# Kernel optimization log

Hardware: AMD Instinct MI355X
Metric: run time of the kernel (lower is better)

The kernel has to match this reference:

```python
import jax, jax.numpy as jnp
import numpy as np

HID, HEADS, FFN = 2048, 16, 8192
HEAD_DIM = HID // HEADS
B, S = 2, 2048
EPS = 1e-5


def setup_inputs() -> dict:
    key = jax.random.key(0)
    ks = jax.random.split(key, 12)
    s = 0.02
    x = jax.random.normal(ks[0], (B, S, HID), dtype=jnp.float32)
    # additive causal mask: 0 on/below diagonal, -inf-like above
    neg = jnp.float32(-1e9)
    causal = jnp.where(jnp.tril(jnp.ones((S, S), dtype=bool)), 0.0, neg)
    mask = causal[None, None, :, :].astype(jnp.float32)
    return {
        "x": x,
        "mask": mask,
        "ln1_w": jnp.ones((HID,), jnp.float32),
        "ln1_b": jnp.zeros((HID,), jnp.float32),
        "q_w": jax.random.normal(ks[1], (HID, HID), jnp.float32) * s,
        "k_w": jax.random.normal(ks[2], (HID, HID), jnp.float32) * s,
        "v_w": jax.random.normal(ks[3], (HID, HID), jnp.float32) * s,
        "o_w": jax.random.normal(ks[4], (HID, HID), jnp.float32) * s,
        "ln2_w": jnp.ones((HID,), jnp.float32),
        "ln2_b": jnp.zeros((HID,), jnp.float32),
        "w1_w": jax.random.normal(ks[5], (FFN, HID), jnp.float32) * s,
        "w1_b": jnp.zeros((FFN,), jnp.float32),
        "wg_w": jax.random.normal(ks[6], (FFN, HID), jnp.float32) * s,
        "w2_w": jax.random.normal(ks[7], (HID, FFN), jnp.float32) * s,
        "w2_b": jnp.zeros((HID,), jnp.float32),
    }


def _layernorm(x, w, b):
    mu = jnp.mean(x, axis=-1, keepdims=True)
    var = jnp.mean(jnp.square(x - mu), axis=-1, keepdims=True)
    return (x - mu) * jax.lax.rsqrt(var + EPS) * w + b


def reference(x, mask, ln1_w, ln1_b, q_w, k_w, v_w, o_w,
              ln2_w, ln2_b, w1_w, w1_b, wg_w, w2_w, w2_b):
    b, s, _ = x.shape
    # --- attention sublayer ---
    h = _layernorm(x, ln1_w, ln1_b)
    def split_heads(y):  # [b,s,hid] -> [b,H,s,d]
        return y.reshape(b, s, HEADS, HEAD_DIM).transpose(0, 2, 1, 3)
    q = split_heads(h @ q_w.T)
    k = split_heads(h @ k_w.T)
    v = split_heads(h @ v_w.T)
    scale = jnp.sqrt(jnp.float32(HEAD_DIM))
    scores = jnp.einsum('bhqd,bhkd->bhqk', q, k) / scale + mask
    weights = jax.nn.softmax(scores, axis=-1)
    attn = jnp.einsum('bhqk,bhkd->bhqd', weights, v)
    attn = attn.transpose(0, 2, 1, 3).reshape(b, s, HID)
    x = x + attn @ o_w.T
    # --- SwiGLU FFN sublayer ---
    h2 = _layernorm(x, ln2_w, ln2_b)
    ff = jax.nn.silu(h2 @ w1_w.T + w1_b) * (h2 @ wg_w.T)
    x = x + ff @ w2_w.T + w2_b
    return x
```

## Files before the change

### kernel.cpp

```cpp
#include <hip/hip_runtime.h>
#include <cstdint>
#include <cstddef>

#define HIDN 2048
#define NROWS 4096
#define FFND 8192
#define SEQ 2048
#define QKVN 6144

typedef __attribute__((ext_vector_type(8))) __bf16 bf16x8;
typedef __attribute__((ext_vector_type(4))) float f32x4;

__device__ __forceinline__ unsigned short f2b(float f) {
    union { float f; unsigned u; } v; v.f = f;
    unsigned r = v.u + 0x7fffu + ((v.u >> 16) & 1u);
    return (unsigned short)(r >> 16);
}
__device__ __forceinline__ float b2f(unsigned short h) {
    union { unsigned u; float f; } v; v.u = ((unsigned)h) << 16; return v.f;
}
__device__ __forceinline__ void gload16(const void* g, void* lds) {
    __builtin_amdgcn_global_load_lds(
        (const __attribute__((address_space(1))) void*)g,
        (__attribute__((address_space(3))) void*)lds, 16, 0, 0);
}

__global__ __launch_bounds__(256) void convall_kernel(
    const float* __restrict__ s0, const float* __restrict__ s1,
    const float* __restrict__ s2, const float* __restrict__ s3,
    const float* __restrict__ s4, const float* __restrict__ s5,
    const float* __restrict__ s6, unsigned short* __restrict__ dst) {
    const int M1 = 1 << 20;
    int i = blockIdx.x * 256 + threadIdx.x;
    const float* src; int rel;
    if      (i <  1 * M1) { src = s0; rel = i;          }
    else if (i <  2 * M1) { src = s1; rel = i - 1 * M1; }
    else if (i <  3 * M1) { src = s2; rel = i - 2 * M1; }
    else if (i <  4 * M1) { src = s3; rel = i - 3 * M1; }
    else if (i <  8 * M1) { src = s4; rel = i - 4 * M1; }
    else if (i < 12 * M1) { src = s5; rel = i - 8 * M1; }
    else                  { src = s6; rel = i - 12 * M1; }
    float4 v = ((const float4*)src)[rel];
    ushort4 o;
    o.x = f2b(v.x); o.y = f2b(v.y); o.z = f2b(v.z); o.w = f2b(v.w);
    ((ushort4*)dst)[i] = o;
}

__global__ __launch_bounds__(256) void ln_kernel(const float* __restrict__ x,
                                                 const float* __restrict__ w,
                                                 const float* __restrict__ b,
                                                 unsigned short* __restrict__ out) {
    int row = blockIdx.x, tid = threadIdx.x;
    const float4* xr = (const float4*)(x + (size_t)row * HIDN);
    float4 a0 = xr[tid], a1 = xr[tid + 256];
    float s  = a0.x + a0.y + a0.z + a0.w + a1.x + a1.y + a1.z + a1.w;
    float s2 = a0.x*a0.x + a0.y*a0.y + a0.z*a0.z + a0.w*a0.w
             + a1.x*a1.x + a1.y*a1.y + a1.z*a1.z + a1.w*a1.w;
#pragma unroll
    for (int i = 1; i < 64; i <<= 1) { s += __shfl_xor(s, i); s2 += __shfl_xor(s2, i); }
    __shared__ float red[8];
    if ((tid & 63) == 0) { red[tid >> 6] = s; red[4 + (tid >> 6)] = s2; }
    __syncthreads();
    s  = red[0] + red[1] + red[2] + red[3];
    s2 = red[4] + red[5] + red[6] + red[7];
    float mu  = s * (1.0f / HIDN);
    float var = s2 * (1.0f / HIDN) - mu * mu;
    float rstd = rsqrtf(var + 1e-5f);
    const float4* wv = (const float4*)w;
    const float4* bv = (const float4*)b;
    float4 w0 = wv[tid], w1 = wv[tid + 256], b0 = bv[tid], b1 = bv[tid + 256];
    ushort4 o0, o1;
    o0.x = f2b((a0.x - mu) * rstd * w0.x + b0.x);
    o0.y = f2b((a0.y - mu) * rstd * w0.y + b0.y);
    o0.z = f2b((a0.z - mu) * rstd * w0.z + b0.z);
    o0.w = f2b((a0.w - mu) * rstd * w0.w + b0.w);
    o1.x = f2b((a1.x - mu) * rstd * w1.x + b1.x);
    o1.y = f2b((a1.y - mu) * rstd * w1.y + b1.y);
    o1.z = f2b((a1.z - mu) * rstd * w1.z + b1.z);
    o1.w = f2b((a1.w - mu) * rstd * w1.w + b1.w);
    ushort4* orow = (ushort4*)(out + (size_t)row * HIDN);
    orow[tid] = o0; orow[tid + 256] = o1;
}

template <int EPI>
__global__ __launch_bounds__(512)
void gemm256(const unsigned short* __restrict__ A, const unsigned short* __restrict__ Bw,
             int M, int N, int K, int tiles_n, float scale,
             const float* __restrict__ bias, const float* __restrict__ resf,
             const unsigned short* __restrict__ aux,
             float* __restrict__ outf, unsigned short* __restrict__ outb) {
    __shared__ unsigned short lds[4][2][8192];
    int tid = threadIdx.x;
    int wave = tid >> 6, lane = tid & 63;
    int lrow = lane & 15, quad = lane >> 4;
    int wm = wave >> 2, wn = wave & 3;
    int nchunk = tiles_n >> 3;
    int xcd = blockIdx.x & 7;
    int pxi = blockIdx.x >> 3;
    int bn = xcd * nchunk + pxi % nchunk;
    int bm = pxi / nchunk;

    f32x4 acc[8][4];
#pragma unroll
    for (int i = 0; i < 8; i++)
#pragma unroll
        for (int j = 0; j < 4; j++) acc[i][j] = f32x4{0.f, 0.f, 0.f, 0.f};

    int srow = wave * 16 + (lane >> 2);
    int scol = (lane & 3) * 8;
    const unsigned short* Ag = A + (size_t)(bm * 256 + srow) * K + scol;
    const unsigned short* Bg = Bw + (size_t)(bn * 256 + srow) * K + scol;
    const int NT = K >> 5;

    auto stage = [&](int slab, int part) {
        const unsigned short* g = part ? Bg : Ag;
        unsigned short* lb = &lds[slab & 3][part][wave * 512];
        size_t koff = (size_t)slab << 5;
        gload16(g + koff, lb);
        gload16(g + koff + (size_t)128 * K, lb + 4096);
    };

    stage(0, 0); stage(0, 1);
    stage(1, 0); stage(1, 1);
    stage(2, 0); stage(2, 1);
    asm volatile("s_waitcnt vmcnt(8)" ::: "memory");
    __builtin_amdgcn_s_barrier();
    asm volatile("" ::: "memory");

#pragma unroll 1
    for (int t = 0; t < NT; ++t) {
        const unsigned short* Abuf = &lds[t & 3][0][0];
        const unsigned short* Bbuf = &lds[t & 3][1][0];
        bf16x8 bfr[4], afr[4];
#pragma unroll
        for (int ni = 0; ni < 4; ni++)
            bfr[ni] = *(const bf16x8*)&Bbuf[(wn * 64 + ni * 16 + lrow) * 32 + quad * 8];
#pragma unroll
        for (int mi = 0; mi < 4; mi++)
            afr[mi] = *(const bf16x8*)&Abuf[(wm * 128 + mi * 16 + lrow) * 32 + quad * 8];
        if (t + 3 < NT) stage(t + 3, 0);
        __builtin_amdgcn_s_barrier();
        asm volatile("s_waitcnt lgkmcnt(0)" ::: "memory");
        __builtin_amdgcn_s_setprio(1);
#pragma unroll
        for (int mi = 0; mi < 4; mi++)
#pragma unroll
            for (int ni = 0; ni < 4; ni++)
                acc[mi][ni] = __builtin_amdgcn_mfma_f32_16x16x32_bf16(afr[mi], bfr[ni], acc[mi][ni], 0, 0, 0);
        __builtin_amdgcn_s_setprio(0);
        __builtin_amdgcn_s_barrier();
        asm volatile("" ::: "memory");
#pragma unroll
        for (int mi = 0; mi < 4; mi++)
            afr[mi] = *(const bf16x8*)&Abuf[(wm * 128 + 64 + mi * 16 + lrow) * 32 + quad * 8];
        if (t + 3 < NT) {
            stage(t + 3, 1);
            asm volatile("s_waitcnt vmcnt(8)" ::: "memory");
        } else if (t + 2 < NT) {
            asm volatile("s_waitcnt vmcnt(4)" ::: "memory");
        } else if (t + 1 < NT) {
            asm volatile("s_waitcnt vmcnt(0)" ::: "memory");
        }
        __builtin_amdgcn_s_barrier();
        asm volatile("s_waitcnt lgkmcnt(0)" ::: "memory");
        __builtin_amdgcn_s_setprio(1);
#pragma unroll
        for (int mi = 0; mi < 4; mi++)
#pragma unroll
            for (int ni = 0; ni < 4; ni++)
                acc[4 + mi][ni] = __builtin_amdgcn_mfma_f32_16x16x32_bf16(afr[mi], bfr[ni], acc[4 + mi][ni], 0, 0, 0);
        __builtin_amdgcn_s_setprio(0);
        __builtin_amdgcn_s_barrier();
        asm volatile("" ::: "memory");
    }

    int row0 = bm * 256 + wm * 128, col0 = bn * 256 + wn * 64;
#pragma unroll
    for (int mi8 = 0; mi8 < 8; mi8++) {
        int rbase = row0 + (mi8 >> 2) * 64 + (mi8 & 3) * 16 + quad * 4;
#pragma unroll
        for (int ni = 0; ni < 4; ni++) {
            int c = col0 + ni * 16 + lrow;
#pragma unroll
            for (int r = 0; r < 4; r++) {
                size_t idx = (size_t)(rbase + r) * N + c;
                float vv = acc[mi8][ni][r];
                if constexpr (EPI == 0) {
                    outb[idx] = f2b(vv * scale);
                } else if constexpr (EPI == 1) {
                    outf[idx] = vv + resf[idx];
                } else if constexpr (EPI == 2) {
                    outb[idx] = f2b(vv + bias[c]);
                } else if constexpr (EPI == 3) {
                    float av = b2f(aux[idx]);
                    float sl = av / (1.f + __expf(-av));
                    outb[idx] = f2b(sl * vv);
                } else if constexpr (EPI == 4) {
                    outf[idx] = vv + bias[c] + resf[idx];
                } else if constexpr (EPI == 5) {
                    outb[idx] = f2b(vv * (c < HIDN ? scale : 1.0f));
                }
            }
        }
    }
    (void)M;
}

__global__ __launch_bounds__(256)
void attn_kernel(const unsigned short* __restrict__ qkv, unsigned short* __restrict__ o) {
    int bh = blockIdx.x;
    int qt = 31 - blockIdx.y;
    int b = bh >> 4, h = bh & 15;
    int tid = threadIdx.x, wave = tid >> 6, lane = tid & 63;
    int lrow = lane & 15, quad = lane >> 4;
    int q0 = qt * 64;
    size_t base = ((size_t)b * SEQ) * QKVN + h * 128;
    const unsigned short* qp0 = qkv + base;
    const unsigned short* kp0 = qkv + base + HIDN;
    const unsigned short* vp0 = qkv + base + 2 * HIDN;
    size_t obase = ((size_t)b * SEQ) * HIDN + h * 128;

    __shared__ unsigned short Ksm[64 * 136];
    __shared__ unsigned short VTsm[128 * 72];
    __shared__ unsigned short Psm[4 * 16 * 72];

    bf16x8 qf[4];
    {
        const unsigned short* qp = qp0 + (size_t)(q0 + wave * 16 + lrow) * QKVN + quad * 8;
#pragma unroll
        for (int kc = 0; kc < 4; kc++) qf[kc] = *(const bf16x8*)(qp + kc * 32);
    }

    f32x4 oacc[8];
#pragma unroll
    for (int i = 0; i < 8; i++) oacc[i] = f32x4{0.f, 0.f, 0.f, 0.f};
    float m_run[4], l_run[4];
    int rowg[4];
#pragma unroll
    for (int r = 0; r < 4; r++) {
        m_run[r] = -1e30f; l_run[r] = 0.f;
        rowg[r] = q0 + wave * 16 + quad * 4 + r;
    }

    for (int kt = 0; kt <= qt; ++kt) {
        {
            int r = tid >> 2, cc = (tid & 3) * 32;
            const uint4* src = (const uint4*)(kp0 + (size_t)(kt * 64 + r) * QKVN + cc);
            uint4* dst = (uint4*)&Ksm[r * 136 + cc];
            dst[0] = src[0]; dst[1] = src[1]; dst[2] = src[2]; dst[3] = src[3];
        }
        {
            int kv = (tid >> 3) * 2, d0 = (tid & 7) * 16;
            const unsigned short* vp = vp0 + (size_t)(kt * 64 + kv) * QKVN + d0;
            unsigned short va[16], vb[16];
            *(uint4*)&va[0] = ((const uint4*)vp)[0];
            *(uint4*)&va[8] = ((const uint4*)vp)[1];
            *(uint4*)&vb[0] = ((const uint4*)(vp + QKVN))[0];
            *(uint4*)&vb[8] = ((const uint4*)(vp + QKVN))[1];
#pragma unroll
            for (int i = 0; i < 16; i++) {
                unsigned pair = (unsigned)va[i] | ((unsigned)vb[i] << 16);
                *(unsigned*)&VTsm[(d0 + i) * 72 + kv] = pair;
            }
        }
        __syncthreads();

        f32x4 sacc[4];
#pragma unroll
        for (int ns = 0; ns < 4; ns++) sacc[ns] = f32x4{0.f, 0.f, 0.f, 0.f};
#pragma unroll
        for (int ns = 0; ns < 4; ns++) {
            const unsigned short* kb = &Ksm[(ns * 16 + lrow) * 136 + quad * 8];
#pragma unroll
            for (int kc = 0; kc < 4; kc++) {
                bf16x8 kf = *(const bf16x8*)(kb + kc * 32);
                sacc[ns] = __builtin_amdgcn_mfma_f32_16x16x32_bf16(qf[kc], kf, sacc[ns], 0, 0, 0);
            }
        }
#pragma unroll
        for (int ns = 0; ns < 4; ns++) {
            int colg = kt * 64 + ns * 16 + lrow;
#pragma unroll
            for (int r = 0; r < 4; r++)
                if (colg > rowg[r]) sacc[ns][r] = -1e30f;
        }
        float mnew[4], alpha[4], rsum[4];
#pragma unroll
        for (int r = 0; r < 4; r++) {
            float mv = fmaxf(fmaxf(sacc[0][r], sacc[1][r]), fmaxf(sacc[2][r], sacc[3][r]));
#pragma unroll
            for (int off = 1; off < 16; off <<= 1) mv = fmaxf(mv, __shfl_xor(mv, off));
            mnew[r] = fmaxf(m_run[r], mv);
            alpha[r] = __expf(m_run[r] - mnew[r]);
            rsum[r] = 0.f;
        }
#pragma unroll
        for (int ns = 0; ns < 4; ns++)
#pragma unroll
            for (int r = 0; r < 4; r++) {
                float p = __expf(sacc[ns][r] - mnew[r]);
                sacc[ns][r] = p;
                rsum[r] += p;
            }
#pragma unroll
        for (int r = 0; r < 4; r++) {
#pragma unroll
            for (int off = 1; off < 16; off <<= 1) rsum[r] += __shfl_xor(rsum[r], off);
            l_run[r] = l_run[r] * alpha[r] + rsum[r];
            m_run[r] = mnew[r];
        }
#pragma unroll
        for (int nc = 0; nc < 8; nc++)
#pragma unroll
            for (int r = 0; r < 4; r++) oacc[nc][r] *= alpha[r];

        unsigned short* pw = &Psm[wave * 16 * 72];
#pragma unroll
        for (int ns = 0; ns < 4; ns++)
#pragma unroll
            for (int r = 0; r < 4; r++)
                pw[(quad * 4 + r) * 72 + ns * 16 + lrow] = f2b(sacc[ns][r]);
        asm volatile("s_waitcnt lgkmcnt(0)" ::: "memory");
        bf16x8 pf[2];
#pragma unroll
        for (int kc = 0; kc < 2; kc++)
            pf[kc] = *(const bf16x8*)&pw[lrow * 72 + kc * 32 + quad * 8];
#pragma unroll
        for (int nc = 0; nc < 8; nc++) {
#pragma unroll
            for (int kc = 0; kc < 2; kc++) {
                bf16x8 vf = *(const bf16x8*)&VTsm[(nc * 16 + lrow) * 72 + kc * 32 + quad * 8];
                oacc[nc] = __builtin_amdgcn_mfma_f32_16x16x32_bf16(pf[kc], vf, oacc[nc], 0, 0, 0);
            }
        }
        __syncthreads();
    }

    float inv[4];
#pragma unroll
    for (int r = 0; r < 4; r++) inv[r] = 1.f / l_run[r];
#pragma unroll
    for (int nc = 0; nc < 8; nc++) {
#pragma unroll
        for (int r = 0; r < 4; r++) {
            int srow = q0 + wave * 16 + quad * 4 + r;
            o[obase + (size_t)srow * HIDN + nc * 16 + lrow] = f2b(oacc[nc][r] * inv[r]);
        }
    }
}

extern "C" void kernel_launch(void* const* d_in, const int* in_sizes, int n_in,
                              void* d_out, int out_size, void* d_ws, size_t ws_size,
                              hipStream_t stream) {
    const float* x    = (const float*)d_in[0];
    const float* ln1w = (const float*)d_in[2];
    const float* ln1b = (const float*)d_in[3];
    const float* qw   = (const float*)d_in[4];
    const float* kw   = (const float*)d_in[5];
    const float* vw   = (const float*)d_in[6];
    const float* ow   = (const float*)d_in[7];
    const float* ln2w = (const float*)d_in[8];
    const float* ln2b = (const float*)d_in[9];
    const float* w1w  = (const float*)d_in[10];
    const float* w1bias = (const float*)d_in[11];
    const float* wgw  = (const float*)d_in[12];
    const float* w2w  = (const float*)d_in[13];
    const float* w2bias = (const float*)d_in[14];
    float* out = (float*)d_out;

    char* ws = (char*)d_ws;
    const size_t MB = 1ull << 20;
    unsigned short* wall  = (unsigned short*)(ws + 0 * MB);
    unsigned short* qkvwb = (unsigned short*)(ws + 0 * MB);
    unsigned short* owb  = (unsigned short*)(ws + 24 * MB);
    unsigned short* w1wb = (unsigned short*)(ws + 32 * MB);
    unsigned short* wgwb = (unsigned short*)(ws + 64 * MB);
    unsigned short* w2wb = (unsigned short*)(ws + 96 * MB);
    unsigned short* a1   = (unsigned short*)(ws + 128 * MB);
    unsigned short* hbuf = (unsigned short*)(ws + 128 * MB);
    unsigned short* qkvb = (unsigned short*)(ws + 144 * MB);
    unsigned short* attnb= (unsigned short*)(ws + 192 * MB);
    unsigned short* h2   = (unsigned short*)(ws + 208 * MB);
    float*          x1   = out;

    convall_kernel<<<65536, 256, 0, stream>>>(qw, kw, vw, ow, w1w, wgw, w2w, wall);

    ln_kernel<<<NROWS, 256, 0, stream>>>(x, ln1w, ln1b, hbuf);

    const float qscale = 0.08838834764831845f;
    gemm256<5><<<dim3(16 * 24), 512, 0, stream>>>(hbuf, qkvwb, NROWS, QKVN, HIDN, 24, qscale,
                                                  nullptr, nullptr, nullptr, nullptr, qkvb);
    attn_kernel<<<dim3(32, 32), 256, 0, stream>>>(qkvb, attnb);
    gemm256<1><<<dim3(16 * 8), 512, 0, stream>>>(attnb, owb, NROWS, HIDN, HIDN, 8, 1.0f,
                                                 nullptr, x, nullptr, x1, nullptr);
    ln_kernel<<<NROWS, 256, 0, stream>>>(x1, ln2w, ln2b, h2);
    gemm256<2><<<dim3(16 * 32), 512, 0, stream>>>(h2, w1wb, NROWS, FFND, HIDN, 32, 1.0f,
                                                  w1bias, nullptr, nullptr, nullptr, a1);
    gemm256<3><<<dim3(16 * 32), 512, 0, stream>>>(h2, wgwb, NROWS, FFND, HIDN, 32, 1.0f,
                                                  nullptr, nullptr, a1, nullptr, a1);
    gemm256<4><<<dim3(16 * 8), 512, 0, stream>>>(a1, w2wb, NROWS, HIDN, FFND, 8, 1.0f,
                                                 w2bias, x1, nullptr, out, nullptr);
    (void)in_sizes; (void)n_in; (void)out_size; (void)ws_size;
}
```

Measured before the change: 1.151 ms.

## Restructure GEMM mainloop to 64-wide K tiles with XOR-swizzled double-buffered LDS

```diff
diff --git a/kernel.cpp b/kernel.cpp
--- a/kernel.cpp
+++ b/kernel.cpp
@@ -89,16 +89,17 @@
              const float* __restrict__ bias, const float* __restrict__ resf,
              const unsigned short* __restrict__ aux,
              float* __restrict__ outf, unsigned short* __restrict__ outb) {
-    __shared__ unsigned short lds[4][2][8192];
-    int tid = threadIdx.x;
-    int wave = tid >> 6, lane = tid & 63;
-    int lrow = lane & 15, quad = lane >> 4;
-    int wm = wave >> 2, wn = wave & 3;
-    int nchunk = tiles_n >> 3;
-    int xcd = blockIdx.x & 7;
-    int pxi = blockIdx.x >> 3;
-    int bn = xcd * nchunk + pxi % nchunk;
-    int bm = pxi / nchunk;
+    __shared__ __align__(16) unsigned short Al[2][256 * 64];
+    __shared__ __align__(16) unsigned short Bl[2][256 * 64];
+    const int tid = threadIdx.x;
+    const int wave = tid >> 6, lane = tid & 63;
+    const int lrow = lane & 15, quad = lane >> 4;
+    const int wm = wave >> 2, wn = wave & 3;
+    const int nchunk = tiles_n >> 3;
+    const int xcd = blockIdx.x & 7;
+    const int pxi = blockIdx.x >> 3;
+    const int bn = xcd * nchunk + pxi % nchunk;
+    const int bm = pxi / nchunk;
 
     f32x4 acc[8][4];
 #pragma unroll
@@ -106,85 +107,139 @@
 #pragma unroll
         for (int j = 0; j < 4; j++) acc[i][j] = f32x4{0.f, 0.f, 0.f, 0.f};
 
-    int srow = wave * 16 + (lane >> 2);
-    int scol = (lane & 3) * 8;
-    const unsigned short* Ag = A + (size_t)(bm * 256 + srow) * K + scol;
-    const unsigned short* Bg = Bw + (size_t)(bn * 256 + srow) * K + scol;
-    const int NT = K >> 5;
-
-    auto stage = [&](int slab, int part) {
-        const unsigned short* g = part ? Bg : Ag;
-        unsigned short* lb = &lds[slab & 3][part][wave * 512];
-        size_t koff = (size_t)slab << 5;
-        gload16(g + koff, lb);
-        gload16(g + koff + (size_t)128 * K, lb + 4096);
+    const int lr8 = lane >> 3;
+    const int colperm = (((lane & 7) ^ lr8) << 3);
+    const int NT = K >> 6;
+
+    const unsigned short* Abase = A + (size_t)(bm * 256) * K;
+    const unsigned short* Bbase = Bw + (size_t)(bn * 256) * K;
+
+    auto stageA = [&](int bufi, int hr, int kt) {
+#pragma unroll
+        for (int j = 0; j < 2; j++) {
+            int ss = wave * 2 + j;
+            int rowbase = hr * 64 + (ss & 7) * 8 + (ss >> 3) * 128;
+            const unsigned short* g = Abase + (size_t)(rowbase + lr8) * K + kt * 64 + colperm;
+            gload16(g, &Al[bufi][rowbase * 64]);
+        }
     };
-
-    stage(0, 0); stage(0, 1);
-    stage(1, 0); stage(1, 1);
-    stage(2, 0); stage(2, 1);
-    asm volatile("s_waitcnt vmcnt(8)" ::: "memory");
+    auto stageB = [&](int bufi, int hr, int kt) {
+#pragma unroll
+        for (int j = 0; j < 2; j++) {
+            int ss = wave * 2 + j;
+            int rowbase = hr * 128 + ss * 8;
+            const unsigned short* g = Bbase + (size_t)(rowbase + lr8) * K + kt * 64 + colperm;
+            gload16(g, &Bl[bufi][rowbase * 64]);
+        }
+    };
+    auto ldA = [&](int bufi, int mf, int kk) -> bf16x8 {
+        int row = wm * 128 + mf * 16 + lrow;
+        int off = row * 64 + ((((kk << 2) | quad) ^ (lrow & 7)) << 3);
+        return *(const bf16x8*)&Al[bufi][off];
+    };
+    auto ldB = [&](int bufi, int nf, int kk) -> bf16x8 {
+        int row = wn * 64 + nf * 16 + lrow;
+        int off = row * 64 + ((((kk << 2) | quad) ^ (lrow & 7)) << 3);
+        return *(const bf16x8*)&Bl[bufi][off];
+    };
+
+    stageB(0, 0, 0); stageB(0, 1, 0); stageA(0, 0, 0); stageA(0, 1, 0);
+    if (NT > 1) {
+        stageB(1, 0, 1); stageB(1, 1, 1); stageA(1, 0, 1);
+        asm volatile("s_waitcnt vmcnt(6)" ::: "memory");
+    } else {
+        asm volatile("s_waitcnt vmcnt(0)" ::: "memory");
+    }
     __builtin_amdgcn_s_barrier();
-    asm volatile("" ::: "memory");
-
+
+    bf16x8 bfr[4][2], afr[2][2];
 #pragma unroll 1
-    for (int t = 0; t < NT; ++t) {
-        const unsigned short* Abuf = &lds[t & 3][0][0];
-        const unsigned short* Bbuf = &lds[t & 3][1][0];
-        bf16x8 bfr[4], afr[4];
-#pragma unroll
-        for (int ni = 0; ni < 4; ni++)
-            bfr[ni] = *(const bf16x8*)&Bbuf[(wn * 64 + ni * 16 + lrow) * 32 + quad * 8];
-#pragma unroll
-        for (int mi = 0; mi < 4; mi++)
-            afr[mi] = *(const bf16x8*)&Abuf[(wm * 128 + mi * 16 + lrow) * 32 + quad * 8];
-        if (t + 3 < NT) stage(t + 3, 0);
+    for (int v = 0; v < NT; ++v) {
+        const int cb = v & 1, nb = cb ^ 1;
+#pragma unroll
+        for (int nf = 0; nf < 4; nf++) { bfr[nf][0] = ldB(cb, nf, 0); bfr[nf][1] = ldB(cb, nf, 1); }
+        afr[0][0] = ldA(cb, 0, 0); afr[0][1] = ldA(cb, 0, 1);
+        afr[1][0] = ldA(cb, 1, 0); afr[1][1] = ldA(cb, 1, 1);
+        if (v + 1 < NT) stageA(nb, 1, v + 1);
+        asm volatile("" ::: "memory");
         __builtin_amdgcn_s_barrier();
         asm volatile("s_waitcnt lgkmcnt(0)" ::: "memory");
         __builtin_amdgcn_s_setprio(1);
 #pragma unroll
-        for (int mi = 0; mi < 4; mi++)
-#pragma unroll
-            for (int ni = 0; ni < 4; ni++)
-                acc[mi][ni] = __builtin_amdgcn_mfma_f32_16x16x32_bf16(afr[mi], bfr[ni], acc[mi][ni], 0, 0, 0);
+        for (int mi = 0; mi < 2; mi++)
+#pragma unroll
+            for (int nf = 0; nf < 4; nf++) {
+                acc[mi][nf] = __builtin_amdgcn_mfma_f32_16x16x32_bf16(afr[mi][0], bfr[nf][0], acc[mi][nf], 0, 0, 0);
+                acc[mi][nf] = __builtin_amdgcn_mfma_f32_16x16x32_bf16(afr[mi][1], bfr[nf][1], acc[mi][nf], 0, 0, 0);
+            }
         __builtin_amdgcn_s_setprio(0);
         __builtin_amdgcn_s_barrier();
+        afr[0][0] = ldA(cb, 2, 0); afr[0][1] = ldA(cb, 2, 1);
+        afr[1][0] = ldA(cb, 3, 0); afr[1][1] = ldA(cb, 3, 1);
+        if (v + 2 < NT) stageB(cb, 0, v + 2);
         asm volatile("" ::: "memory");
-#pragma unroll
-        for (int mi = 0; mi < 4; mi++)
-            afr[mi] = *(const bf16x8*)&Abuf[(wm * 128 + 64 + mi * 16 + lrow) * 32 + quad * 8];
-        if (t + 3 < NT) {
-            stage(t + 3, 1);
-            asm volatile("s_waitcnt vmcnt(8)" ::: "memory");
-        } else if (t + 2 < NT) {
-            asm volatile("s_waitcnt vmcnt(4)" ::: "memory");
-        } else if (t + 1 < NT) {
-            asm volatile("s_waitcnt vmcnt(0)" ::: "memory");
-        }
         __builtin_amdgcn_s_barrier();
         asm volatile("s_waitcnt lgkmcnt(0)" ::: "memory");
         __builtin_amdgcn_s_setprio(1);
 #pragma unroll
-        for (int mi = 0; mi < 4; mi++)
-#pragma unroll
-            for (int ni = 0; ni < 4; ni++)
-                acc[4 + mi][ni] = __builtin_amdgcn_mfma_f32_16x16x32_bf16(afr[mi], bfr[ni], acc[4 + mi][ni], 0, 0, 0);
+        for (int mi = 0; mi < 2; mi++)
+#pragma unroll
+            for (int nf = 0; nf < 4; nf++) {
+                acc[2 + mi][nf] = __builtin_amdgcn_mfma_f32_16x16x32_bf16(afr[mi][0], bfr[nf][0], acc[2 + mi][nf], 0, 0, 0);
+                acc[2 + mi][nf] = __builtin_amdgcn_mfma_f32_16x16x32_bf16(afr[mi][1], bfr[nf][1], acc[2 + mi][nf], 0, 0, 0);
+            }
         __builtin_amdgcn_s_setprio(0);
         __builtin_amdgcn_s_barrier();
+        afr[0][0] = ldA(cb, 4, 0); afr[0][1] = ldA(cb, 4, 1);
+        afr[1][0] = ldA(cb, 5, 0); afr[1][1] = ldA(cb, 5, 1);
+        if (v + 2 < NT) stageB(cb, 1, v + 2);
         asm volatile("" ::: "memory");
+        __builtin_amdgcn_s_barrier();
+        asm volatile("s_waitcnt lgkmcnt(0)" ::: "memory");
+        __builtin_amdgcn_s_setprio(1);
+#pragma unroll
+        for (int mi = 0; mi < 2; mi++)
+#pragma unroll
+            for (int nf = 0; nf < 4; nf++) {
+                acc[4 + mi][nf] = __builtin_amdgcn_mfma_f32_16x16x32_bf16(afr[mi][0], bfr[nf][0], acc[4 + mi][nf], 0, 0, 0);
+                acc[4 + mi][nf] = __builtin_amdgcn_mfma_f32_16x16x32_bf16(afr[mi][1], bfr[nf][1], acc[4 + mi][nf], 0, 0, 0);
+            }
+        __builtin_amdgcn_s_setprio(0);
+        __builtin_amdgcn_s_barrier();
+        afr[0][0] = ldA(cb, 6, 0); afr[0][1] = ldA(cb, 6, 1);
+        afr[1][0] = ldA(cb, 7, 0); afr[1][1] = ldA(cb, 7, 1);
+        if (v + 2 < NT) {
+            stageA(cb, 0, v + 2);
+            asm volatile("s_waitcnt vmcnt(6)" ::: "memory");
+        } else if (v + 1 < NT) {
+            asm volatile("s_waitcnt vmcnt(0)" ::: "memory");
+        }
+        asm volatile("" ::: "memory");
+        __builtin_amdgcn_s_barrier();
+        asm volatile("s_waitcnt lgkmcnt(0)" ::: "memory");
+        __builtin_amdgcn_s_setprio(1);
+#pragma unroll
+        for (int mi = 0; mi < 2; mi++)
+#pragma unroll
+            for (int nf = 0; nf < 4; nf++) {
+                acc[6 + mi][nf] = __builtin_amdgcn_mfma_f32_16x16x32_bf16(afr[mi][0], bfr[nf][0], acc[6 + mi][nf], 0, 0, 0);
+                acc[6 + mi][nf] = __builtin_amdgcn_mfma_f32_16x16x32_bf16(afr[mi][1], bfr[nf][1], acc[6 + mi][nf], 0, 0, 0);
+            }
+        __builtin_amdgcn_s_setprio(0);
+        __builtin_amdgcn_s_barrier();
     }
 
     int row0 = bm * 256 + wm * 128, col0 = bn * 256 + wn * 64;
 #pragma unroll
-    for (int mi8 = 0; mi8 < 8; mi8++) {
-        int rbase = row0 + (mi8 >> 2) * 64 + (mi8 & 3) * 16 + quad * 4;
-#pragma unroll
-        for (int ni = 0; ni < 4; ni++) {
-            int c = col0 + ni * 16 + lrow;
+    for (int mf = 0; mf < 8; mf++) {
+#pragma unroll
+        for (int nf = 0; nf < 4; nf++) {
+            int c = col0 + nf * 16 + lrow;
 #pragma unroll
             for (int r = 0; r < 4; r++) {
-                size_t idx = (size_t)(rbase + r) * N + c;
-                float vv = acc[mi8][ni][r];
+                int rr = row0 + mf * 16 + quad * 4 + r;
+                size_t idx = (size_t)rr * N + c;
+                float vv = acc[mf][nf][r];
                 if constexpr (EPI == 0) {
                     outb[idx] = f2b(vv * scale);
                 } else if constexpr (EPI == 1) {
```

Result: faster. 1.091 ms (-5.2%).
